# Optimization experiments

Measured on AMD Instinct MI355X. Metric: run time of the kernel, lower is better.

The kernel has to match this reference:

```python
import jax, jax.numpy as jnp
import numpy as np


def setup_inputs() -> dict:
    key = jax.random.key(0)
    k1, k2 = jax.random.split(key)
    # x: (B, C, D, H, W); w: (out_ch, C * 2*2*2)
    x = jax.random.normal(k1, (4, 64, 33, 33, 33), dtype=jnp.float32)
    w = jax.random.normal(k2, (128, 64 * 8), dtype=jnp.float32) * 0.05
    return {"x": x, "w": w}


def reference(x, w):
    # unfoldNd(kernel=2, stride=1, pad=0) + einsum('ij,kjm->kim', w, patches)
    # is exactly a valid 3D cross-correlation with a 2x2x2 kernel.
    B, C, D, H, W = x.shape
    O = w.shape[0]
    kern = w.reshape(O, C, 2, 2, 2)  # unfold flattening order: (C, kd, kh, kw)
    y = jax.lax.conv_general_dilated(
        x, kern,
        window_strides=(1, 1, 1),
        padding='VALID',
        dimension_numbers=('NCDHW', 'OIDHW', 'NCDHW'),
    )  # (B, O, D-1, H-1, W-1)
    return (y + 1.0) ** 2
```

## Files before the change

### kernel.cpp

```cpp
#include <hip/hip_runtime.h>

typedef __bf16 bf16x8 __attribute__((ext_vector_type(8)));
typedef float f32x4 __attribute__((ext_vector_type(4)));
typedef float f32x16 __attribute__((ext_vector_type(16)));
typedef unsigned short u16;
typedef unsigned int u32;
typedef u32 u32x4 __attribute__((ext_vector_type(4)));
typedef u16 u16x8 __attribute__((ext_vector_type(8)));

#define AS1 __attribute__((address_space(1)))
#define AS3 __attribute__((address_space(3)))
#define GLL16(gp, lp) __builtin_amdgcn_global_load_lds((const AS1 void*)(gp), (AS3 void*)(lp), 16, 0, 0)

__device__ __forceinline__ u16 f32_to_bf16_rne(float f) {
    union { float f; unsigned u; } cv; cv.f = f;
    unsigned u = cv.u;
    return (u16)((u + 0x7FFFu + ((u >> 16) & 1u)) >> 16);
}

__device__ __forceinline__ u32 cvt_pk_bf16(float lo, float hi) {
    u32 r;
    asm("v_cvt_pk_bf16_f32 %0, %1, %2" : "=v"(r) : "v"(lo), "v"(hi));
    return r;
}

__global__ __launch_bounds__(256) void prepass_kernel(
    const float* __restrict__ x, const float* __restrict__ w,
    u16* __restrict__ xT, u16* __restrict__ x32, u16* __restrict__ w4) {

    const int bid = blockIdx.x;
    const int tid = threadIdx.x;

    if (bid < 4356) {
        const int h = bid % 33;
        const int dq = bid / 33;
        const int d = dq % 33;
        const int b = dq / 33;
        const float* xp = x + (size_t)b * 2299968 + d * 1089 + h * 33;

        const int wv  = tid & 31;
        const int cc  = tid >> 5;
        const float* p = xp + (size_t)cc * 8 * 35937 + wv;
        float f0 = p[0],              f1 = p[35937],          f2 = p[2 * 35937], f3 = p[3 * 35937];
        float f4 = p[(size_t)4*35937],f5 = p[(size_t)5*35937],f6 = p[(size_t)6*35937],f7 = p[(size_t)7*35937];
        u32x4 v;
        v[0] = cvt_pk_bf16(f0, f1);
        v[1] = cvt_pk_bf16(f2, f3);
        v[2] = cvt_pk_bf16(f4, f5);
        v[3] = cvt_pk_bf16(f6, f7);
        *reinterpret_cast<u32x4*>(&xT[(size_t)bid * 2048 + cc * 256 + wv * 8]) = v;

        if (tid < 8) {
            const float* q = xp + (size_t)tid * 8 * 35937 + 32;
            u32x4 m;
            m[0] = cvt_pk_bf16(q[0],              q[35937]);
            m[1] = cvt_pk_bf16(q[2 * 35937],      q[3 * 35937]);
            m[2] = cvt_pk_bf16(q[(size_t)4*35937],q[(size_t)5*35937]);
            m[3] = cvt_pk_bf16(q[(size_t)6*35937],q[(size_t)7*35937]);
            *reinterpret_cast<u32x4*>(&x32[(size_t)bid * 64 + tid * 8]) = m;
        }
    } else {
        int e = (bid - 4356) * 256 + tid;
        int j    = e & 7;
        int half = (e >> 3) & 1;
        int o    = (e >> 4) & 127;
        int cq   = (e >> 11) & 3;
        int koff = (e >> 13) & 7;
        int c = cq * 16 + half * 8 + j;
        w4[e] = f32_to_bf16_rne(w[(o << 9) + (c << 3) + koff]);
    }
}

__global__ void repack_w_kernel(const float* __restrict__ w, u16* __restrict__ w3) {
    int e = blockIdx.x * 256 + threadIdx.x;
    int j    = e & 7;
    int g    = (e >> 3) & 3;
    int o    = (e >> 5) & 127;
    int cb   = (e >> 12) & 1;
    int koff = (e >> 13) & 7;
    int c = (cb << 5) + (g << 3) + j;
    w3[e] = f32_to_bf16_rne(w[(o << 9) + (c << 3) + koff]);
}

__global__ __launch_bounds__(512, 4) void conv_mfma_kernel(
    const u16* __restrict__ xT, const u16* __restrict__ x32,
    const u16* __restrict__ w4, float* __restrict__ out) {

    __shared__ __align__(16) u16 xs[38016];

    const int tid  = threadIdx.x;
    const int bid0 = blockIdx.x;
    const int wgid = ((bid0 & 7) << 6) + (bid0 >> 3);
    const int b    = wgid >> 7;
    const int dz   = (wgid >> 2) & 31;
    const int hy0  = (wgid & 3) << 3;

    char* ldsb = (char*)xs;
    const int slab0 = b * 1089 + dz * 33 + hy0;
#pragma unroll
    for (int r = 0; r < 9; ++r) {
        const int u   = tid + (r << 9);
        const int sid = u >> 8;
        const int kd  = sid >= 9;
        const int hh  = sid - kd * 9;
        const char* src = (const char*)xT + ((size_t)(slab0 + kd * 33 + hh) << 12)
                          + ((u & 255) << 4);
        GLL16(src, ldsb + (u << 4));
    }
    if (tid < 144) {
        const int sid = tid >> 3;
        const int kd  = sid >= 9;
        const int hh  = sid - kd * 9;
        const char* src = (const char*)x32
            + ((size_t)(slab0 + kd * 33 + hh) << 7) + ((tid & 7) << 4);
        GLL16(src, ldsb + 73728 + (tid << 4));
    }
    asm volatile("s_waitcnt vmcnt(0)" ::: "memory");
    __syncthreads();

    const int lane = tid & 63;
    const int l31  = lane & 31;
    const int half = lane >> 5;
    const int wid  = tid >> 6;
    const int o0   = (wid & 3) << 5;
    const int hb   = (wid >> 2) << 2;

    f32x16 acc[4];
#pragma unroll
    for (int ht = 0; ht < 4; ++ht)
#pragma unroll
        for (int r = 0; r < 16; ++r)
            acc[ht][r] = 0.f;

#pragma unroll
    for (int kw = 0; kw < 2; ++kw) {
        const int row = l31 + kw;
#pragma unroll
        for (int cq = 0; cq < 4; ++cq) {
            const int cc = (cq << 1) + half;
            bf16x8 A[2][2];
#pragma unroll
            for (int kd = 0; kd < 2; ++kd)
#pragma unroll
                for (int kh = 0; kh < 2; ++kh) {
                    const int t = (((kd << 2) + (kh << 1) + kw) << 2) + cq;
                    const u16* p = w4 + (t << 11) + ((o0 + l31) << 4) + (half << 3);
                    A[kd][kh] = __builtin_bit_cast(bf16x8, *reinterpret_cast<const u16x8*>(p));
                }
            bf16x8 Bc[2], Bn[2];
#pragma unroll
            for (int kd = 0; kd < 2; ++kd) {
                const int sid = kd * 9 + hb;
                const u16* p = (row < 32)
                    ? &xs[(sid << 11) + (cc << 8) + (row << 3)]
                    : &xs[36864 + (sid << 6) + (cc << 3)];
                Bc[kd] = __builtin_bit_cast(bf16x8, *reinterpret_cast<const u16x8*>(p));
            }
#pragma unroll
            for (int ht = 0; ht < 4; ++ht) {
#pragma unroll
                for (int kd = 0; kd < 2; ++kd) {
                    const int sid = kd * 9 + hb + ht + 1;
                    const u16* p = (row < 32)
                        ? &xs[(sid << 11) + (cc << 8) + (row << 3)]
                        : &xs[36864 + (sid << 6) + (cc << 3)];
                    Bn[kd] = __builtin_bit_cast(bf16x8, *reinterpret_cast<const u16x8*>(p));
                }
#pragma unroll
                for (int kd = 0; kd < 2; ++kd) {
                    acc[ht] = __builtin_amdgcn_mfma_f32_32x32x16_bf16(
                        A[kd][0], Bc[kd], acc[ht], 0, 0, 0);
                    acc[ht] = __builtin_amdgcn_mfma_f32_32x32x16_bf16(
                        A[kd][1], Bn[kd], acc[ht], 0, 0, 0);
                }
                Bc[0] = Bn[0];
                Bc[1] = Bn[1];
            }
        }
    }

    float* ob = out + (size_t)b * 128 * 32768 + ((size_t)dz << 10)
                + ((hy0 + hb) << 5) + l31;
#pragma unroll
    for (int r = 0; r < 16; ++r) {
        const int orow = (r & 3) + ((r >> 2) << 3) + (half << 2);
        float* o2 = ob + ((size_t)(o0 + orow) << 15);
#pragma unroll
        for (int ht = 0; ht < 4; ++ht) {
            float v = acc[ht][r] + 1.0f;
            o2[ht << 5] = v * v;
        }
    }
}

#define XS_ROW 72
__global__ __launch_bounds__(256, 4) void conv_mfma_fallback(
    const float* __restrict__ x, const u16* __restrict__ w3, float* __restrict__ out) {

    __shared__ __align__(16) u16 xs[6 * 33 * XS_ROW];

    const int tid = threadIdx.x;
    const int bid = blockIdx.x;
    const int hy0 = (bid & 15) << 1;
    const int dz  = (bid >> 4) & 31;
    const int b   = bid >> 9;

    const float* xb = x + (size_t)b * 64 * 35937;
    for (int i = tid; i < 1584; i += 256) {
        int w   = i % 33;
        int t   = i / 33;
        int q   = t & 7;
        int kh3 = t >> 3;
        int kd  = kh3 >= 3 ? 1 : 0;
        int kh  = kh3 - kd * 3;
        const float* p = xb + (size_t)(q << 3) * 35937 + (dz + kd) * 1089 + (hy0 + kh) * 33 + w;
        u32x4 v;
        v[0] = cvt_pk_bf16(p[0], p[35937]);
        v[1] = cvt_pk_bf16(p[2 * 35937], p[3 * 35937]);
        v[2] = cvt_pk_bf16(p[4 * 35937], p[5 * 35937]);
        v[3] = cvt_pk_bf16(p[6 * 35937], p[7 * 35937]);
        *reinterpret_cast<u32x4*>(&xs[(kh3 * 33 + w) * XS_ROW + (q << 3)]) = v;
    }
    __syncthreads();

    const int lane = tid & 63;
    const int ln   = lane & 15;
    const int g    = lane >> 4;
    const int n0w  = (tid >> 6) << 5;

    f32x4 acc[2][4];
#pragma unroll
    for (int nf = 0; nf < 2; ++nf)
#pragma unroll
        for (int mf = 0; mf < 4; ++mf)
            acc[nf][mf] = (f32x4){0.f, 0.f, 0.f, 0.f};

#pragma unroll
    for (int cb = 0; cb < 2; ++cb) {
        const int cbase = (cb << 5) + (g << 3);
#pragma unroll
        for (int kd = 0; kd < 2; ++kd) {
            bf16x8 wf[2][4];
#pragma unroll
            for (int nf = 0; nf < 2; ++nf)
#pragma unroll
                for (int kk = 0; kk < 4; ++kk) {
                    const int koff = (kd << 2) + kk;
                    const u16* p = w3 + (size_t)((((koff << 1) + cb) << 7)
                                   + n0w + (nf << 4) + ln) * 32 + (g << 3);
                    wf[nf][kk] = __builtin_bit_cast(bf16x8, *reinterpret_cast<const u16x8*>(p));
                }
#pragma unroll
            for (int kw = 0; kw < 2; ++kw) {
                bf16x8 xf[3][2];
#pragma unroll
                for (int hh = 0; hh < 3; ++hh)
#pragma unroll
                    for (int wh = 0; wh < 2; ++wh) {
                        const int rw = (kd * 3 + hh) * 33 + (wh << 4) + ln + kw;
                        xf[hh][wh] = __builtin_bit_cast(bf16x8,
                            *reinterpret_cast<const u16x8*>(&xs[rw * XS_ROW + cbase]));
                    }
#pragma unroll
                for (int kh = 0; kh < 2; ++kh)
#pragma unroll
                    for (int nf = 0; nf < 2; ++nf)
#pragma unroll
                        for (int mf = 0; mf < 4; ++mf)
                            acc[nf][mf] = __builtin_amdgcn_mfma_f32_16x16x32_bf16(
                                wf[nf][(kh << 1) + kw], xf[(mf >> 1) + kh][mf & 1],
                                acc[nf][mf], 0, 0, 0);
            }
        }
    }

    float* ob = out + ((size_t)b * 128) * 32768 + (dz << 10) + (hy0 << 5);
#pragma unroll
    for (int nf = 0; nf < 2; ++nf)
#pragma unroll
        for (int mf = 0; mf < 4; ++mf) {
            const int wx   = ((mf & 1) << 4) + ln;
            const int hrow = mf >> 1;
            float* o2 = ob + (hrow << 5) + wx;
#pragma unroll
            for (int r = 0; r < 4; ++r) {
                const int n = n0w + (nf << 4) + (g << 2) + r;
                float v = acc[nf][mf][r] + 1.0f;
                o2[(size_t)n << 15] = v * v;
            }
        }
}

extern "C" void kernel_launch(void* const* d_in, const int* in_sizes, int n_in,
                              void* d_out, int out_size, void* d_ws, size_t ws_size,
                              hipStream_t stream) {
    const float* x = (const float*)d_in[0];
    const float* w = (const float*)d_in[1];
    float* out = (float*)d_out;

    const size_t W_BYTES   = 131072;
    const size_t XT_BYTES  = (size_t)4356 * 4096;
    const size_t X32_BYTES = (size_t)4356 * 128;
    const size_t NEED = W_BYTES + XT_BYTES + X32_BYTES;

    if (ws_size >= NEED) {
        u16* w4  = (u16*)d_ws;
        u16* xT  = (u16*)((char*)d_ws + W_BYTES);
        u16* x32 = (u16*)((char*)d_ws + W_BYTES + XT_BYTES);
        prepass_kernel<<<4612, 256, 0, stream>>>(x, w, xT, x32, w4);
        conv_mfma_kernel<<<512, 512, 0, stream>>>(xT, x32, w4, out);
    } else {
        u16* w3 = (u16*)d_ws;
        repack_w_kernel<<<256, 256, 0, stream>>>(w, w3);
        conv_mfma_fallback<<<2048, 256, 0, stream>>>(x, w3, out);
    }
}
```

Measured before the change: 43.61 us.

## Double-buffer LDS tiles per block and remap tiles to 2 dz x 4 hy

Each workgroup now handles two output tiles, each covering 2 dz slices by 4 hy rows, instead of one tile of 1 dz by 8 hy rows. The second tile's slab is loaded asynchronously into a second LDS buffer while the first tile's MFMAs run, so the load latency is hidden. The tile shape change alters halo reuse: 3x5 slabs per tile instead of 2x9. The costs are half as many blocks (256 on a large GPU), double the LDS per block, and a lower occupancy bound, which may leave CUs idle.

```diff
diff --git a/kernel.cpp b/kernel.cpp
--- a/kernel.cpp
+++ b/kernel.cpp
@@ -82,48 +82,17 @@
     w3[e] = f32_to_bf16_rne(w[(o << 9) + (c << 3) + koff]);
 }
 
-__global__ __launch_bounds__(512, 4) void conv_mfma_kernel(
-    const u16* __restrict__ xT, const u16* __restrict__ x32,
-    const u16* __restrict__ w4, float* __restrict__ out) {
-
-    __shared__ __align__(16) u16 xs[38016];
-
-    const int tid  = threadIdx.x;
-    const int bid0 = blockIdx.x;
-    const int wgid = ((bid0 & 7) << 6) + (bid0 >> 3);
-    const int b    = wgid >> 7;
-    const int dz   = (wgid >> 2) & 31;
-    const int hy0  = (wgid & 3) << 3;
-
-    char* ldsb = (char*)xs;
-    const int slab0 = b * 1089 + dz * 33 + hy0;
-#pragma unroll
-    for (int r = 0; r < 9; ++r) {
-        const int u   = tid + (r << 9);
-        const int sid = u >> 8;
-        const int kd  = sid >= 9;
-        const int hh  = sid - kd * 9;
-        const char* src = (const char*)xT + ((size_t)(slab0 + kd * 33 + hh) << 12)
-                          + ((u & 255) << 4);
-        GLL16(src, ldsb + (u << 4));
-    }
-    if (tid < 144) {
-        const int sid = tid >> 3;
-        const int kd  = sid >= 9;
-        const int hh  = sid - kd * 9;
-        const char* src = (const char*)x32
-            + ((size_t)(slab0 + kd * 33 + hh) << 7) + ((tid & 7) << 4);
-        GLL16(src, ldsb + 73728 + (tid << 4));
-    }
-    asm volatile("s_waitcnt vmcnt(0)" ::: "memory");
-    __syncthreads();
+
+__device__ __forceinline__ void process_tile(
+    const u16* __restrict__ buf, const u16* __restrict__ w4,
+    float* __restrict__ out, int b, int dz0, int hy0, int tid) {
 
     const int lane = tid & 63;
     const int l31  = lane & 31;
     const int half = lane >> 5;
     const int wid  = tid >> 6;
+    const int od   = wid >> 2;
     const int o0   = (wid & 3) << 5;
-    const int hb   = (wid >> 2) << 2;
 
     f32x16 acc[4];
 #pragma unroll
@@ -150,20 +119,20 @@
             bf16x8 Bc[2], Bn[2];
 #pragma unroll
             for (int kd = 0; kd < 2; ++kd) {
-                const int sid = kd * 9 + hb;
+                const int sid = (od + kd) * 5;
                 const u16* p = (row < 32)
-                    ? &xs[(sid << 11) + (cc << 8) + (row << 3)]
-                    : &xs[36864 + (sid << 6) + (cc << 3)];
+                    ? &buf[(sid << 11) + (cc << 8) + (row << 3)]
+                    : &buf[30720 + (sid << 6) + (cc << 3)];
                 Bc[kd] = __builtin_bit_cast(bf16x8, *reinterpret_cast<const u16x8*>(p));
             }
 #pragma unroll
             for (int ht = 0; ht < 4; ++ht) {
 #pragma unroll
                 for (int kd = 0; kd < 2; ++kd) {
-                    const int sid = kd * 9 + hb + ht + 1;
+                    const int sid = (od + kd) * 5 + ht + 1;
                     const u16* p = (row < 32)
-                        ? &xs[(sid << 11) + (cc << 8) + (row << 3)]
-                        : &xs[36864 + (sid << 6) + (cc << 3)];
+                        ? &buf[(sid << 11) + (cc << 8) + (row << 3)]
+                        : &buf[30720 + (sid << 6) + (cc << 3)];
                     Bn[kd] = __builtin_bit_cast(bf16x8, *reinterpret_cast<const u16x8*>(p));
                 }
 #pragma unroll
@@ -179,8 +148,9 @@
         }
     }
 
+    const int dz = dz0 + od;
     float* ob = out + (size_t)b * 128 * 32768 + ((size_t)dz << 10)
-                + ((hy0 + hb) << 5) + l31;
+                + (hy0 << 5) + l31;
 #pragma unroll
     for (int r = 0; r < 16; ++r) {
         const int orow = (r & 3) + ((r >> 2) << 3) + (half << 2);
@@ -191,6 +161,64 @@
             o2[ht << 5] = v * v;
         }
     }
+}
+
+__device__ __forceinline__ void stage_tile(
+    const u16* __restrict__ xT, const u16* __restrict__ x32,
+    u16* __restrict__ buf, int b, int dz0, int hy0, int tid) {
+
+    char* ldsb = (char*)buf;
+    const int slab0 = b * 1089 + dz0 * 33 + hy0;
+#pragma unroll
+    for (int r = 0; r < 8; ++r) {
+        if (r == 7 && tid >= 256) continue;
+        const int u   = tid + (r << 9);
+        const int sid = u >> 8;
+        const int S   = (sid * 205) >> 10;
+        const int hh  = sid - S * 5;
+        const char* src = (const char*)xT + ((size_t)(slab0 + S * 33 + hh) << 12)
+                          + ((u & 255) << 4);
+        GLL16(src, ldsb + (u << 4));
+    }
+    if (tid < 120) {
+        const int sid = tid >> 3;
+        const int S   = (sid * 205) >> 10;
+        const int hh  = sid - S * 5;
+        const char* src = (const char*)x32
+            + ((size_t)(slab0 + S * 33 + hh) << 7) + ((tid & 7) << 4);
+        GLL16(src, ldsb + 61440 + (tid << 4));
+    }
+}
+
+__global__ __launch_bounds__(512, 2) void conv_mfma_kernel(
+    const u16* __restrict__ xT, const u16* __restrict__ x32,
+    const u16* __restrict__ w4, float* __restrict__ out) {
+
+    __shared__ __align__(16) u16 xs[2][31680];
+
+    const int tid  = threadIdx.x;
+    const int bid0 = blockIdx.x;
+    const int wgid = ((bid0 & 7) << 5) + (bid0 >> 3);
+    const int hyq  = wgid & 7;
+    const int r2   = wgid >> 3;
+    const int dzq  = r2 & 7;
+    const int b    = r2 >> 3;
+    const int hy0  = hyq << 2;
+    const int dzA  = (dzq << 2);
+    const int dzB  = dzA + 2;
+
+    stage_tile(xT, x32, xs[0], b, dzA, hy0, tid);
+    asm volatile("s_waitcnt vmcnt(0)" ::: "memory");
+    __syncthreads();
+
+    stage_tile(xT, x32, xs[1], b, dzB, hy0, tid);
+
+    process_tile(xs[0], w4, out, b, dzA, hy0, tid);
+
+    asm volatile("s_waitcnt vmcnt(0)" ::: "memory");
+    __syncthreads();
+
+    process_tile(xs[1], w4, out, b, dzB, hy0, tid);
 }
 
 #define XS_ROW 72
@@ -308,7 +336,7 @@
         u16* xT  = (u16*)((char*)d_ws + W_BYTES);
         u16* x32 = (u16*)((char*)d_ws + W_BYTES + XT_BYTES);
         prepass_kernel<<<4612, 256, 0, stream>>>(x, w, xT, x32, w4);
-        conv_mfma_kernel<<<512, 512, 0, stream>>>(xT, x32, w4, out);
+        conv_mfma_kernel<<<256, 512, 0, stream>>>(xT, x32, w4, out);
     } else {
         u16* w3 = (u16*)d_ws;
         repack_w_kernel<<<256, 256, 0, stream>>>(w, w3);
```

Measured after the change: 46.32 us. 1.06x slower.
